# Kernel optimization log

Measured on AMD Instinct MI355X. Metric: run time of the kernel, lower is better.

Reference implementation:

```python
import jax, jax.numpy as jnp
import numpy as np

B, T, F, H = 4096, 60, 128, 256

def setup_inputs() -> dict:
    key = jax.random.key(0)
    ks = jax.random.split(key, 14)
    sk = 1.0 / np.sqrt(H)
    def unif(k, shape):
        return jax.random.uniform(k, shape, jnp.float32, -sk, sk)
    return {
        "x": jax.random.normal(ks[0], (B, T, F), jnp.float32),
        "Wf": unif(ks[1], (F + H, H)), "bf": unif(ks[2], (H,)),
        "Wu": unif(ks[3], (F + H, H)), "bu": unif(ks[4], (H,)),
        "Wc": unif(ks[5], (F + H, H)), "bc": unif(ks[6], (H,)),
        "Wo": unif(ks[7], (F + H, H)), "bo": unif(ks[8], (H,)),
        "Wd1": jax.random.normal(ks[9], (H, H), jnp.float32) * np.sqrt(2.0 / H),
        "bd1": jnp.zeros((H,), jnp.float32),
        "Wd2": jax.random.normal(ks[10], (H, 1), jnp.float32) * np.sqrt(2.0 / H),
        "bd2": jnp.zeros((1,), jnp.float32),
    }

def reference(x, Wf, bf, Wu, bu, Wc, bc, Wo, bo, Wd1, bd1, Wd2, bd2):
    b = x.shape[0]
    h0 = jnp.zeros((b, H), x.dtype)
    c0 = jnp.zeros((b, H), x.dtype)

    def step(carry, xt):
        h, c = carry
        z = jnp.concatenate([xt, h], axis=-1)  # [B, F+H]
        f = jax.nn.sigmoid(z @ Wf + bf)
        u = jax.nn.sigmoid(z @ Wu + bu)
        g = jnp.tanh(z @ Wc + bc)
        o = jax.nn.sigmoid(z @ Wo + bo)
        c_new = f * c + u * g
        h_new = o * jnp.tanh(c_new)
        return (h_new, c_new), None

    (h, _), _ = jax.lax.scan(step, (h0, c0), jnp.swapaxes(x, 0, 1))  # scan over T
    # dense head: two stacked linear layers, no intermediate activation
    out = (h @ Wd1 + bd1) @ Wd2 + bd2  # [B, 1]
    return out
```

## Files before the change

### kernel.cpp

```cpp
#include <hip/hip_runtime.h>


#define T_STEPS 60
#define F_DIM 128
#define H_DIM 256
#define BC 16
#define ZQ 31.75f
#define L2E 1.44269504f

typedef __attribute__((ext_vector_type(4))) int intx4;

__device__ __forceinline__ int q8(float v) {
    return __float2int_rn(fminf(fmaxf(v, -127.f), 127.f));
}

__global__ void colmax_kernel(const float* __restrict__ Wf, const float* __restrict__ Wu,
                              const float* __restrict__ Wc, const float* __restrict__ Wo,
                              float* __restrict__ cscale, float* __restrict__ fh) {
    __shared__ float red[4][64];
    int t = threadIdx.x;
    int g = blockIdx.x >> 2, cg = blockIdx.x & 3;
    const float* W = (g == 0) ? Wf : (g == 1) ? Wu : (g == 2) ? Wc : Wo;
    int col = cg * 64 + (t & 63);
    int s = t >> 6;
    const int k0s[4] = {0, 64, 128, 256};
    const int ns[4]  = {64, 64, 128, 128};
    float m = 1e-20f;
    for (int i = 0; i < ns[s]; ++i)
        m = fmaxf(m, fabsf(W[(size_t)(k0s[s] + i) * H_DIM + col]));
    red[s][t & 63] = m;
    __syncthreads();
    if (t < 64) {
        float Mx = fmaxf(red[0][t], red[1][t]);
        float Mh = fmaxf(red[2][t], red[3][t]);
        float cs = fmaxf(4.f * Mx, Mh) * (1.f / (127.f * 127.f));
        int j = g * 256 + cg * 64 + t;
        cscale[j] = cs;
        fh[j] = 1.f / (127.f * cs);
    }
}

__global__ void pack_q_kernel(const float* __restrict__ Wf, const float* __restrict__ Wu,
                              const float* __restrict__ Wc, const float* __restrict__ Wo,
                              const float* __restrict__ fh, intx4* __restrict__ qpack) {
    __shared__ float wst[64 * 256];
    int t = threadIdx.x;
    int ks6 = blockIdx.x % 6, g = blockIdx.x / 6;
    const float* W = (g == 0) ? Wf : (g == 1) ? Wu : (g == 2) ? Wc : Wo;
#pragma unroll
    for (int i = 0; i < 16; ++i) {
        int row = i * 4 + (t >> 6);
        int c4 = (t & 63) * 4;
        *(float4*)(wst + row * 256 + c4) =
            *(const float4*)(W + (size_t)(ks6 * 64 + row) * H_DIM + c4);
    }
    __syncthreads();
    float fb = (ks6 < 2) ? 4.f : 1.f;
#pragma unroll
    for (int i = 0; i < 4; ++i) {
        int task = i * 256 + t;
        int lane = task & 63, hblk = task >> 6;
        int l15 = lane & 15, quad = lane >> 4;
        int col = hblk * 16 + l15;
        int k0 = quad * 16;
        float f = fb * fh[g * 256 + col];
        int w[4];
#pragma unroll
        for (int d = 0; d < 4; ++d) {
            int b0 = q8(wst[(k0 + d * 4 + 0) * 256 + col] * f) & 255;
            int b1 = q8(wst[(k0 + d * 4 + 1) * 256 + col] * f) & 255;
            int b2 = q8(wst[(k0 + d * 4 + 2) * 256 + col] * f) & 255;
            int b3 = q8(wst[(k0 + d * 4 + 3) * 256 + col] * f) & 255;
            w[d] = b0 | (b1 << 8) | (b2 << 16) | (b3 << 24);
        }
        intx4 v = {w[0], w[1], w[2], w[3]};
        qpack[((hblk * 4 + g) * 6 + ks6) * 64 + lane] = v;
    }
}

__global__ void head_prep_kernel(const float* __restrict__ Wd1, const float* __restrict__ bd1,
                                 const float* __restrict__ Wd2, const float* __restrict__ bd2,
                                 float* __restrict__ vhead, float* __restrict__ shead) {
    __shared__ float hp[256];
    int t = threadIdx.x;
    int j = blockIdx.x * 64 + (t >> 2);
    int q = t & 3;
    float s = 0.f;
    const float* row = Wd1 + (size_t)j * H_DIM + q * 64;
#pragma unroll
    for (int i = 0; i < 16; ++i) {
        float4 a = *(const float4*)(row + i * 4);
        float4 b = *(const float4*)(Wd2 + q * 64 + i * 4);
        s += a.x * b.x + a.y * b.y + a.z * b.z + a.w * b.w;
    }
    hp[t] = s;
    __syncthreads();
    if ((t & 3) == 0)
        vhead[j] = hp[t] + hp[t + 1] + hp[t + 2] + hp[t + 3];
    if (blockIdx.x == 0) {
        __syncthreads();
        hp[t] = bd1[t] * Wd2[t];
        __syncthreads();
        for (int off = 128; off > 0; off >>= 1) {
            if (t < off) hp[t] += hp[t + off];
            __syncthreads();
        }
        if (t == 0) shead[0] = hp[0] + bd2[0];
    }
}

__global__ __launch_bounds__(512)
__attribute__((amdgpu_waves_per_eu(2, 2)))
void lstm_kernel(const float* __restrict__ x,
                 const float* __restrict__ bfv, const float* __restrict__ buv,
                 const float* __restrict__ bcv, const float* __restrict__ bov,
                 const intx4* __restrict__ qpack,
                 const float* __restrict__ cscale,
                 const float* __restrict__ vhead, const float* __restrict__ shead,
                 float* __restrict__ out)
{
    __shared__ __align__(16) signed char wlds[2 * 64 * 64 * 16];
    __shared__ __align__(16) signed char zbuf[2][6][1024];
    __shared__ float rowsum[BC];

    const int tid  = threadIdx.x;
    const int wave = tid >> 6;
    const int lane = tid & 63;
    const int quad = lane >> 4;
    const int l15  = lane & 15;
    const int b0   = blockIdx.x * BC;

    for (int i = tid; i < 2 * 64 * 64; i += 512) {
        int ks4 = i >> 12, nt = (i >> 6) & 63, ln = i & 63;
        ((intx4*)wlds)[i] = qpack[(nt * 6 + 4 + ks4) * 64 + ln];
    }
    intx4 wreg[4][8];
#pragma unroll
    for (int j = 0; j < 8; ++j)
#pragma unroll
        for (int ks = 0; ks < 4; ++ks) {
            intx4 v = qpack[(((8 * wave + j) * 6 + ks) * 64) + lane];
            int a0 = v[0], a1 = v[1], a2 = v[2], a3 = v[3];
            asm volatile("" : "+v"(a0), "+v"(a1), "+v"(a2), "+v"(a3));
            intx4 w = {a0, a1, a2, a3};
            wreg[ks][j] = w;
        }

    for (int i = tid; i < 2 * 6 * 1024 / 4; i += 512) ((int*)zbuf)[i] = 0;
    if (tid < BC) rowsum[tid] = 0.f;

    float csS[2][4], bS[2][4], vh[2];
    float creg[2][4] = {};
    int haddr[2];
#pragma unroll
    for (int hb = 0; hb < 2; ++hb) {
        int a = 2 * wave + hb;
        int hc = a * 16 + l15;
        vh[hb] = vhead[hc];
        haddr[hb] = (2 + (a >> 2)) * 1024 + (a & 3) * 256 + l15;
#pragma unroll
        for (int g = 0; g < 4; ++g) {
            float cs = cscale[g * 256 + hc];
            float bi = (g == 0 ? bfv : g == 1 ? buv : g == 2 ? bcv : bov)[hc];
            float m = (g == 2) ? (-2.f * L2E) : (-L2E);
            csS[hb][g] = m * cs;
            bS[hb][g] = m * bi;
        }
    }

    const int xm = tid >> 5, xi = tid & 31;
    const int f0 = xi * 4;
    const int xaddr = (f0 >> 6) * 1024 + ((f0 & 63) >> 4) * 256 + xm * 16 + (f0 & 15);
    const float* xp = x + (size_t)(b0 + xm) * T_STEPS * F_DIM + f0;

    __syncthreads();
    float4 xv = *(const float4*)(xp);
    {
        unsigned u = (unsigned)(q8(xv.x * ZQ) & 255) | ((unsigned)(q8(xv.y * ZQ) & 255) << 8) |
                     ((unsigned)(q8(xv.z * ZQ) & 255) << 16) | ((unsigned)(q8(xv.w * ZQ) & 255) << 24);
        *(unsigned*)(&zbuf[0][0][0] + xaddr) = u;
    }
    xv = *(const float4*)(xp + F_DIM);
    __syncthreads();

    for (int t = 0; t < T_STEPS; ++t) {
        const int p = t & 1, pn = p ^ 1;
        const signed char* zr = &zbuf[p][0][0];
        signed char* zw = &zbuf[pn][0][0];

        intx4 af[6];
#pragma unroll
        for (int ks = 0; ks < 6; ++ks)
            af[ks] = *(const intx4*)(zr + ks * 1024 + lane * 16);

        intx4 acc[8] = {};
#pragma unroll
        for (int ks = 0; ks < 4; ++ks)
#pragma unroll
            for (int j = 0; j < 8; ++j)
                acc[j] = __builtin_amdgcn_mfma_i32_16x16x64_i8(af[ks], wreg[ks][j], acc[j], 0, 0, 0);
#pragma unroll
        for (int k4 = 0; k4 < 2; ++k4)
#pragma unroll
            for (int j = 0; j < 8; ++j) {
                intx4 b = ((const intx4*)wlds)[(k4 * 64 + 8 * wave + j) * 64 + lane];
                acc[j] = __builtin_amdgcn_mfma_i32_16x16x64_i8(af[4 + k4], b, acc[j], 0, 0, 0);
            }

        if (t < T_STEPS - 1) {
            unsigned u = (unsigned)(q8(xv.x * ZQ) & 255) | ((unsigned)(q8(xv.y * ZQ) & 255) << 8) |
                         ((unsigned)(q8(xv.z * ZQ) & 255) << 16) | ((unsigned)(q8(xv.w * ZQ) & 255) << 24);
            *(unsigned*)(zw + xaddr) = u;
            if (t < T_STEPS - 2)
                xv = *(const float4*)(xp + (size_t)(t + 2) * F_DIM);

#pragma unroll
            for (int hb = 0; hb < 2; ++hb)
#pragma unroll
                for (int rr = 0; rr < 4; ++rr) {
                    float uf = fmaf((float)acc[hb * 4 + 0][rr], csS[hb][0], bS[hb][0]);
                    float uu = fmaf((float)acc[hb * 4 + 1][rr], csS[hb][1], bS[hb][1]);
                    float uc = fmaf((float)acc[hb * 4 + 2][rr], csS[hb][2], bS[hb][2]);
                    float uo = fmaf((float)acc[hb * 4 + 3][rr], csS[hb][3], bS[hb][3]);
                    float fg = __builtin_amdgcn_rcpf(1.f + __builtin_amdgcn_exp2f(uf));
                    float ug = __builtin_amdgcn_rcpf(1.f + __builtin_amdgcn_exp2f(uu));
                    float rc = __builtin_amdgcn_rcpf(1.f + __builtin_amdgcn_exp2f(uc));
                    float og = __builtin_amdgcn_rcpf(1.f + __builtin_amdgcn_exp2f(uo));
                    float cn = fmaf(fg, creg[hb][rr], fmaf(ug + ug, rc, -ug));
                    creg[hb][rr] = cn;
                    float rh = __builtin_amdgcn_rcpf(1.f + __builtin_amdgcn_exp2f(cn * (-2.f * L2E)));
                    float hn = fmaf(og + og, rh, -og);
                    zw[haddr[hb] + (quad * 4 + rr) * 16] =
                        (signed char)__float2int_rn(hn * 127.f);
                }
        } else {
            float hs[4] = {0.f, 0.f, 0.f, 0.f};
#pragma unroll
            for (int hb = 0; hb < 2; ++hb)
#pragma unroll
                for (int rr = 0; rr < 4; ++rr) {
                    float uf = fmaf((float)acc[hb * 4 + 0][rr], csS[hb][0], bS[hb][0]);
                    float uu = fmaf((float)acc[hb * 4 + 1][rr], csS[hb][1], bS[hb][1]);
                    float uc = fmaf((float)acc[hb * 4 + 2][rr], csS[hb][2], bS[hb][2]);
                    float uo = fmaf((float)acc[hb * 4 + 3][rr], csS[hb][3], bS[hb][3]);
                    float fg = __builtin_amdgcn_rcpf(1.f + __builtin_amdgcn_exp2f(uf));
                    float ug = __builtin_amdgcn_rcpf(1.f + __builtin_amdgcn_exp2f(uu));
                    float rc = __builtin_amdgcn_rcpf(1.f + __builtin_amdgcn_exp2f(uc));
                    float og = __builtin_amdgcn_rcpf(1.f + __builtin_amdgcn_exp2f(uo));
                    float cn = fmaf(fg, creg[hb][rr], fmaf(ug + ug, rc, -ug));
                    float rh = __builtin_amdgcn_rcpf(1.f + __builtin_amdgcn_exp2f(cn * (-2.f * L2E)));
                    float hn = fmaf(og + og, rh, -og);
                    hs[rr] += hn * vh[hb];
                }
#pragma unroll
            for (int rr = 0; rr < 4; ++rr) {
                float s = hs[rr];
#pragma unroll
                for (int m = 1; m < 16; m <<= 1)
                    s += __shfl_xor(s, m, 64);
                if (l15 == 0)
                    atomicAdd(&rowsum[quad * 4 + rr], s);
            }
        }
        __syncthreads();
    }

    if (tid < BC)
        out[b0 + tid] = rowsum[tid] + shead[0];
}

extern "C" void kernel_launch(void* const* d_in, const int* in_sizes, int n_in,
                              void* d_out, int out_size, void* d_ws, size_t ws_size,
                              hipStream_t stream) {
    (void)in_sizes; (void)n_in; (void)out_size; (void)ws_size;
    const float* x   = (const float*)d_in[0];
    const float* Wf  = (const float*)d_in[1];
    const float* bfv = (const float*)d_in[2];
    const float* Wu  = (const float*)d_in[3];
    const float* buv = (const float*)d_in[4];
    const float* Wc  = (const float*)d_in[5];
    const float* bcv = (const float*)d_in[6];
    const float* Wo  = (const float*)d_in[7];
    const float* bov = (const float*)d_in[8];
    const float* Wd1 = (const float*)d_in[9];
    const float* bd1 = (const float*)d_in[10];
    const float* Wd2 = (const float*)d_in[11];
    const float* bd2 = (const float*)d_in[12];

    char* ws = (char*)d_ws;
    intx4* qpack = (intx4*)ws;
    size_t off = (size_t)384 * 64 * 16;
    float* cscale = (float*)(ws + off); off += 1024 * 4;
    float* fh     = (float*)(ws + off); off += 1024 * 4;
    float* vhead  = (float*)(ws + off); off += 256 * 4;
    float* shead  = (float*)(ws + off); off += 16;

    colmax_kernel<<<16, 256, 0, stream>>>(Wf, Wu, Wc, Wo, cscale, fh);
    pack_q_kernel<<<24, 256, 0, stream>>>(Wf, Wu, Wc, Wo, fh, qpack);
    head_prep_kernel<<<4, 256, 0, stream>>>(Wd1, bd1, Wd2, bd2, vhead, shead);
    lstm_kernel<<<256, 512, 0, stream>>>(x, bfv, buv, bcv, bov, qpack, cscale,
                                         vhead, shead, (float*)d_out);
}
```

Before: 333.2 us.

## Fuse prep kernels, keep five weight K-slices in registers, pair sigmoid reciprocals

The three weight-preparation kernels (column max, int8 quantize-pack, head folding) become a single 9-block launch, which removes two kernel launches and the intermediate scale buffer. In the LSTM kernel, one more K-slice of the quantized weights (five of six) is held in VGPRs, so only one slice is streamed from LDS per step, and the A-fragments are loaded per slice rather than all up front. The gate sigmoids now share reciprocals in pairs (one rcp per two gates plus extra multiplies). The cost is higher register pressure that could cause spills at 2 waves/EU, and a slightly different rounding path for the gates.

```diff
diff --git a/kernel.cpp b/kernel.cpp
--- a/kernel.cpp
+++ b/kernel.cpp
@@ -14,92 +14,83 @@
     return __float2int_rn(fminf(fmaxf(v, -127.f), 127.f));
 }
 
-__global__ void colmax_kernel(const float* __restrict__ Wf, const float* __restrict__ Wu,
-                              const float* __restrict__ Wc, const float* __restrict__ Wo,
-                              float* __restrict__ cscale, float* __restrict__ fh) {
-    __shared__ float red[4][64];
-    int t = threadIdx.x;
-    int g = blockIdx.x >> 2, cg = blockIdx.x & 3;
-    const float* W = (g == 0) ? Wf : (g == 1) ? Wu : (g == 2) ? Wc : Wo;
-    int col = cg * 64 + (t & 63);
-    int s = t >> 6;
-    const int k0s[4] = {0, 64, 128, 256};
-    const int ns[4]  = {64, 64, 128, 128};
-    float m = 1e-20f;
-    for (int i = 0; i < ns[s]; ++i)
-        m = fmaxf(m, fabsf(W[(size_t)(k0s[s] + i) * H_DIM + col]));
-    red[s][t & 63] = m;
-    __syncthreads();
-    if (t < 64) {
-        float Mx = fmaxf(red[0][t], red[1][t]);
-        float Mh = fmaxf(red[2][t], red[3][t]);
-        float cs = fmaxf(4.f * Mx, Mh) * (1.f / (127.f * 127.f));
-        int j = g * 256 + cg * 64 + t;
-        cscale[j] = cs;
-        fh[j] = 1.f / (127.f * cs);
-    }
-}
-
-__global__ void pack_q_kernel(const float* __restrict__ Wf, const float* __restrict__ Wu,
-                              const float* __restrict__ Wc, const float* __restrict__ Wo,
-                              const float* __restrict__ fh, intx4* __restrict__ qpack) {
-    __shared__ float wst[64 * 256];
-    int t = threadIdx.x;
-    int ks6 = blockIdx.x % 6, g = blockIdx.x / 6;
-    const float* W = (g == 0) ? Wf : (g == 1) ? Wu : (g == 2) ? Wc : Wo;
-#pragma unroll
-    for (int i = 0; i < 16; ++i) {
-        int row = i * 4 + (t >> 6);
-        int c4 = (t & 63) * 4;
-        *(float4*)(wst + row * 256 + c4) =
-            *(const float4*)(W + (size_t)(ks6 * 64 + row) * H_DIM + c4);
-    }
-    __syncthreads();
-    float fb = (ks6 < 2) ? 4.f : 1.f;
-#pragma unroll
-    for (int i = 0; i < 4; ++i) {
-        int task = i * 256 + t;
-        int lane = task & 63, hblk = task >> 6;
-        int l15 = lane & 15, quad = lane >> 4;
-        int col = hblk * 16 + l15;
-        int k0 = quad * 16;
-        float f = fb * fh[g * 256 + col];
-        int w[4];
-#pragma unroll
-        for (int d = 0; d < 4; ++d) {
-            int b0 = q8(wst[(k0 + d * 4 + 0) * 256 + col] * f) & 255;
-            int b1 = q8(wst[(k0 + d * 4 + 1) * 256 + col] * f) & 255;
-            int b2 = q8(wst[(k0 + d * 4 + 2) * 256 + col] * f) & 255;
-            int b3 = q8(wst[(k0 + d * 4 + 3) * 256 + col] * f) & 255;
-            w[d] = b0 | (b1 << 8) | (b2 << 16) | (b3 << 24);
-        }
-        intx4 v = {w[0], w[1], w[2], w[3]};
-        qpack[((hblk * 4 + g) * 6 + ks6) * 64 + lane] = v;
-    }
-}
-
-__global__ void head_prep_kernel(const float* __restrict__ Wd1, const float* __restrict__ bd1,
-                                 const float* __restrict__ Wd2, const float* __restrict__ bd2,
-                                 float* __restrict__ vhead, float* __restrict__ shead) {
-    __shared__ float hp[256];
-    int t = threadIdx.x;
-    int j = blockIdx.x * 64 + (t >> 2);
-    int q = t & 3;
-    float s = 0.f;
-    const float* row = Wd1 + (size_t)j * H_DIM + q * 64;
-#pragma unroll
-    for (int i = 0; i < 16; ++i) {
-        float4 a = *(const float4*)(row + i * 4);
-        float4 b = *(const float4*)(Wd2 + q * 64 + i * 4);
-        s += a.x * b.x + a.y * b.y + a.z * b.z + a.w * b.w;
-    }
-    hp[t] = s;
-    __syncthreads();
-    if ((t & 3) == 0)
-        vhead[j] = hp[t] + hp[t + 1] + hp[t + 2] + hp[t + 3];
-    if (blockIdx.x == 0) {
-        __syncthreads();
-        hp[t] = bd1[t] * Wd2[t];
+__global__ __launch_bounds__(1024)
+void prep_kernel(const float* __restrict__ Wf, const float* __restrict__ Wu,
+                 const float* __restrict__ Wc, const float* __restrict__ Wo,
+                 const float* __restrict__ Wd1, const float* __restrict__ bd1,
+                 const float* __restrict__ Wd2, const float* __restrict__ bd2,
+                 float* __restrict__ cscale, intx4* __restrict__ qpack,
+                 float* __restrict__ vhead, float* __restrict__ shead) {
+    const int t = threadIdx.x;
+    const int b = blockIdx.x;
+    if (b < 8) {
+        __shared__ float red[16][128];
+        __shared__ float fsc[128];
+        const int g = b >> 1, ch = b & 1;
+        const float* W = (g == 0) ? Wf : (g == 1) ? Wu : (g == 2) ? Wc : Wo;
+        const int col = ch * 128 + (t & 127);
+        const int grp = t >> 7;
+        float mx = 1e-20f, mh = 1e-20f;
+#pragma unroll 4
+        for (int i = 0; i < 16; ++i)
+            mx = fmaxf(mx, fabsf(W[(size_t)(grp * 16 + i) * H_DIM + col]));
+#pragma unroll 4
+        for (int i = 0; i < 32; ++i)
+            mh = fmaxf(mh, fabsf(W[(size_t)(128 + grp * 32 + i) * H_DIM + col]));
+        red[grp][t & 127] = mx;
+        red[8 + grp][t & 127] = mh;
+        __syncthreads();
+        if (t < 128) {
+            float Mx = red[0][t], Mh = red[8][t];
+#pragma unroll
+            for (int i = 1; i < 8; ++i) {
+                Mx = fmaxf(Mx, red[i][t]);
+                Mh = fmaxf(Mh, red[8 + i][t]);
+            }
+            float cs = fmaxf(4.f * Mx, Mh) * (1.f / 16129.f);
+            cscale[g * 256 + ch * 128 + t] = cs;
+            fsc[t] = 1.f / (127.f * cs);
+        }
+        __syncthreads();
+#pragma unroll
+        for (int i = 0; i < 3; ++i) {
+            int task = i * 1024 + t;
+            int lane = task & 63, fr = task >> 6;
+            int hl = fr / 6, ks6 = fr - hl * 6;
+            int l15 = lane & 15, quad = lane >> 4;
+            int colw = ch * 128 + hl * 16 + l15;
+            int k0 = ks6 * 64 + quad * 16;
+            float f = ((ks6 < 2) ? 4.f : 1.f) * fsc[hl * 16 + l15];
+            int w[4];
+#pragma unroll
+            for (int d = 0; d < 4; ++d) {
+                int b0 = q8(W[(size_t)(k0 + d * 4 + 0) * H_DIM + colw] * f) & 255;
+                int b1 = q8(W[(size_t)(k0 + d * 4 + 1) * H_DIM + colw] * f) & 255;
+                int b2 = q8(W[(size_t)(k0 + d * 4 + 2) * H_DIM + colw] * f) & 255;
+                int b3 = q8(W[(size_t)(k0 + d * 4 + 3) * H_DIM + colw] * f) & 255;
+                w[d] = b0 | (b1 << 8) | (b2 << 16) | (b3 << 24);
+            }
+            intx4 v = {w[0], w[1], w[2], w[3]};
+            qpack[(((ch * 8 + hl) * 4 + g) * 6 + ks6) * 64 + lane] = v;
+        }
+    } else {
+        __shared__ float hp[1024];
+        const int j = t >> 2, q = t & 3;
+        float s = 0.f;
+        const float* row = Wd1 + (size_t)j * H_DIM + q * 64;
+#pragma unroll
+        for (int i = 0; i < 16; ++i) {
+            float4 a = *(const float4*)(row + i * 4);
+            float4 bb = *(const float4*)(Wd2 + q * 64 + i * 4);
+            s += a.x * bb.x + a.y * bb.y + a.z * bb.z + a.w * bb.w;
+        }
+        hp[t] = s;
+        __syncthreads();
+        float vj = 0.f;
+        if (q == 0) vj = hp[t] + hp[t + 1] + hp[t + 2] + hp[t + 3];
+        __syncthreads();
+        if (q == 0) vhead[j] = vj;
+        if (t < 256) hp[t] = bd1[t] * Wd2[t];
         __syncthreads();
         for (int off = 128; off > 0; off >>= 1) {
             if (t < off) hp[t] += hp[t + off];
@@ -119,7 +110,7 @@
                  const float* __restrict__ vhead, const float* __restrict__ shead,
                  float* __restrict__ out)
 {
-    __shared__ __align__(16) signed char wlds[2 * 64 * 64 * 16];
+    __shared__ __align__(16) intx4 wlds[64 * 64];
     __shared__ __align__(16) signed char zbuf[2][6][1024];
     __shared__ float rowsum[BC];
 
@@ -130,15 +121,13 @@
     const int l15  = lane & 15;
     const int b0   = blockIdx.x * BC;
 
-    for (int i = tid; i < 2 * 64 * 64; i += 512) {
-        int ks4 = i >> 12, nt = (i >> 6) & 63, ln = i & 63;
-        ((intx4*)wlds)[i] = qpack[(nt * 6 + 4 + ks4) * 64 + ln];
-    }
-    intx4 wreg[4][8];
+    for (int i = tid; i < 64 * 64; i += 512)
+        wlds[i] = qpack[((i >> 6) * 6 + 5) * 64 + (i & 63)];
+    intx4 wreg[5][8];
 #pragma unroll
     for (int j = 0; j < 8; ++j)
 #pragma unroll
-        for (int ks = 0; ks < 4; ++ks) {
+        for (int ks = 0; ks < 5; ++ks) {
             intx4 v = qpack[(((8 * wave + j) * 6 + ks) * 64) + lane];
             int a0 = v[0], a1 = v[1], a2 = v[2], a3 = v[3];
             asm volatile("" : "+v"(a0), "+v"(a1), "+v"(a2), "+v"(a3));
@@ -185,27 +174,25 @@
 
     for (int t = 0; t < T_STEPS; ++t) {
         const int p = t & 1, pn = p ^ 1;
-        const signed char* zr = &zbuf[p][0][0];
+        const intx4* zr = (const intx4*)(&zbuf[p][0][0]);
         signed char* zw = &zbuf[pn][0][0];
 
-        intx4 af[6];
-#pragma unroll
-        for (int ks = 0; ks < 6; ++ks)
-            af[ks] = *(const intx4*)(zr + ks * 1024 + lane * 16);
-
         intx4 acc[8] = {};
 #pragma unroll
-        for (int ks = 0; ks < 4; ++ks)
+        for (int ks = 0; ks < 5; ++ks) {
+            intx4 a = zr[ks * 64 + lane];
 #pragma unroll
             for (int j = 0; j < 8; ++j)
-                acc[j] = __builtin_amdgcn_mfma_i32_16x16x64_i8(af[ks], wreg[ks][j], acc[j], 0, 0, 0);
-#pragma unroll
-        for (int k4 = 0; k4 < 2; ++k4)
+                acc[j] = __builtin_amdgcn_mfma_i32_16x16x64_i8(a, wreg[ks][j], acc[j], 0, 0, 0);
+        }
+        {
+            intx4 a5 = zr[5 * 64 + lane];
 #pragma unroll
             for (int j = 0; j < 8; ++j) {
-                intx4 b = ((const intx4*)wlds)[(k4 * 64 + 8 * wave + j) * 64 + lane];
-                acc[j] = __builtin_amdgcn_mfma_i32_16x16x64_i8(af[4 + k4], b, acc[j], 0, 0, 0);
+                intx4 bw = wlds[(8 * wave + j) * 64 + lane];
+                acc[j] = __builtin_amdgcn_mfma_i32_16x16x64_i8(a5, bw, acc[j], 0, 0, 0);
             }
+        }
 
         if (t < T_STEPS - 1) {
             unsigned u = (unsigned)(q8(xv.x * ZQ) & 255) | ((unsigned)(q8(xv.y * ZQ) & 255) << 8) |
@@ -222,10 +209,16 @@
                     float uu = fmaf((float)acc[hb * 4 + 1][rr], csS[hb][1], bS[hb][1]);
                     float uc = fmaf((float)acc[hb * 4 + 2][rr], csS[hb][2], bS[hb][2]);
                     float uo = fmaf((float)acc[hb * 4 + 3][rr], csS[hb][3], bS[hb][3]);
-                    float fg = __builtin_amdgcn_rcpf(1.f + __builtin_amdgcn_exp2f(uf));
-                    float ug = __builtin_amdgcn_rcpf(1.f + __builtin_amdgcn_exp2f(uu));
-                    float rc = __builtin_amdgcn_rcpf(1.f + __builtin_amdgcn_exp2f(uc));
-                    float og = __builtin_amdgcn_rcpf(1.f + __builtin_amdgcn_exp2f(uo));
+                    float af = 1.f + __builtin_amdgcn_exp2f(uf);
+                    float au = 1.f + __builtin_amdgcn_exp2f(uu);
+                    float ac = 1.f + __builtin_amdgcn_exp2f(uc);
+                    float ao = 1.f + __builtin_amdgcn_exp2f(uo);
+                    float r1 = __builtin_amdgcn_rcpf(af * au);
+                    float r2 = __builtin_amdgcn_rcpf(ac * ao);
+                    float fg = au * r1;
+                    float ug = af * r1;
+                    float rc = ao * r2;
+                    float og = ac * r2;
                     float cn = fmaf(fg, creg[hb][rr], fmaf(ug + ug, rc, -ug));
                     creg[hb][rr] = cn;
                     float rh = __builtin_amdgcn_rcpf(1.f + __builtin_amdgcn_exp2f(cn * (-2.f * L2E)));
@@ -243,10 +236,16 @@
                     float uu = fmaf((float)acc[hb * 4 + 1][rr], csS[hb][1], bS[hb][1]);
                     float uc = fmaf((float)acc[hb * 4 + 2][rr], csS[hb][2], bS[hb][2]);
                     float uo = fmaf((float)acc[hb * 4 + 3][rr], csS[hb][3], bS[hb][3]);
-                    float fg = __builtin_amdgcn_rcpf(1.f + __builtin_amdgcn_exp2f(uf));
-                    float ug = __builtin_amdgcn_rcpf(1.f + __builtin_amdgcn_exp2f(uu));
-                    float rc = __builtin_amdgcn_rcpf(1.f + __builtin_amdgcn_exp2f(uc));
-                    float og = __builtin_amdgcn_rcpf(1.f + __builtin_amdgcn_exp2f(uo));
+                    float af = 1.f + __builtin_amdgcn_exp2f(uf);
+                    float au = 1.f + __builtin_amdgcn_exp2f(uu);
+                    float ac = 1.f + __builtin_amdgcn_exp2f(uc);
+                    float ao = 1.f + __builtin_amdgcn_exp2f(uo);
+                    float r1 = __builtin_amdgcn_rcpf(af * au);
+                    float r2 = __builtin_amdgcn_rcpf(ac * ao);
+                    float fg = au * r1;
+                    float ug = af * r1;
+                    float rc = ao * r2;
+                    float og = ac * r2;
                     float cn = fmaf(fg, creg[hb][rr], fmaf(ug + ug, rc, -ug));
                     float rh = __builtin_amdgcn_rcpf(1.f + __builtin_amdgcn_exp2f(cn * (-2.f * L2E)));
                     float hn = fmaf(og + og, rh, -og);
@@ -291,13 +290,11 @@
     intx4* qpack = (intx4*)ws;
     size_t off = (size_t)384 * 64 * 16;
     float* cscale = (float*)(ws + off); off += 1024 * 4;
-    float* fh     = (float*)(ws + off); off += 1024 * 4;
     float* vhead  = (float*)(ws + off); off += 256 * 4;
     float* shead  = (float*)(ws + off); off += 16;
 
-    colmax_kernel<<<16, 256, 0, stream>>>(Wf, Wu, Wc, Wo, cscale, fh);
-    pack_q_kernel<<<24, 256, 0, stream>>>(Wf, Wu, Wc, Wo, fh, qpack);
-    head_prep_kernel<<<4, 256, 0, stream>>>(Wd1, bd1, Wd2, bd2, vhead, shead);
+    prep_kernel<<<9, 1024, 0, stream>>>(Wf, Wu, Wc, Wo, Wd1, bd1, Wd2, bd2,
+                                        cscale, qpack, vhead, shead);
     lstm_kernel<<<256, 512, 0, stream>>>(x, bfv, buv, bcv, bov, qpack, cscale,
                                          vhead, shead, (float*)d_out);
 }
```

Result: faster. 307.6 us (-7.7%).
